# Kernel optimization log

Measured on AMD Instinct MI355X. Metric: run time of the kernel, lower is better.

Reference implementation:

```python
import jax, jax.numpy as jnp
import numpy as np


def setup_inputs() -> dict:
    key = jax.random.key(0)
    k1, k2, k3 = jax.random.split(key, 3)
    x = jax.random.normal(k1, (32, 256, 64, 64), dtype=jnp.float32)
    w = jax.random.normal(k2, (1, 1, 7, 7), dtype=jnp.float32) * (1.0 / 7.0)
    b = jax.random.normal(k3, (1,), dtype=jnp.float32) * 0.1
    return {"x": x, "w": w, "b": b}


def reference(x, w, b):
    # channel-wise mean and max pooling, keepdim -> [B,1,H,W]
    pooled = jnp.mean(x, axis=1, keepdims=True) + jnp.max(x, axis=1, keepdims=True)
    # 7x7 conv, 1->1 channel, SAME padding (pad=3)
    attn = jax.lax.conv_general_dilated(
        pooled, w,
        window_strides=(1, 1),
        padding=((3, 3), (3, 3)),
        dimension_numbers=("NCHW", "OIHW", "NCHW"),
    ) + b[None, :, None, None]
    attn = jax.nn.sigmoid(attn)
    return x * attn  # broadcast over channels
```

## Files before the change

kernel.cpp:

```cpp
#include <hip/hip_runtime.h>
#include <math.h>

#define BATCH 32
#define CH    256
#define HH    64
#define WW    64
#define HW    (HH * WW)
#define NPIX  (BATCH * HW)
#define PG    (NPIX / 4)
#define NTOT  ((size_t)BATCH * CH * HW)
#define NCHUNK 4
#define CCHUNK (CH / NCHUNK)

typedef float floatx4 __attribute__((ext_vector_type(4)));

__global__ __launch_bounds__(256) void sa_pool_partial(
    const float* __restrict__ x,
    float4* __restrict__ pSum, float4* __restrict__ pMax) {
    int t = blockIdx.x * 256 + threadIdx.x;
    int pg    = t & (PG - 1);
    int chunk = t >> 15;
    int b   = pg >> 10;
    int hwg = pg & 1023;
    const float4* p = reinterpret_cast<const float4*>(
        x + (size_t)b * CH * HW + (size_t)chunk * CCHUNK * HW) + hwg;
    float4 s = make_float4(0.f, 0.f, 0.f, 0.f);
    float4 m = make_float4(-INFINITY, -INFINITY, -INFINITY, -INFINITY);
#pragma unroll 8
    for (int c = 0; c < CCHUNK; ++c) {
        float4 v = p[c * (HW / 4)];
        s.x += v.x; s.y += v.y; s.z += v.z; s.w += v.w;
        m.x = fmaxf(m.x, v.x); m.y = fmaxf(m.y, v.y);
        m.z = fmaxf(m.z, v.z); m.w = fmaxf(m.w, v.w);
    }
    pSum[chunk * PG + pg] = s;
    pMax[chunk * PG + pg] = m;
}

__global__ __launch_bounds__(256) void sa_comb_conv(
    const float4* __restrict__ pSum, const float4* __restrict__ pMax,
    const float* __restrict__ wgt, const float* __restrict__ bias,
    float* __restrict__ attn) {
    __shared__ float pooled[22][64];
    __shared__ float wq[49];
    int bidx = blockIdx.x;
    int b = bidx >> 2;
    int s = bidx & 3;
    int t = threadIdx.x;
    if (t < 49) wq[t] = wgt[t];
    int rowbase = 16 * s - 3; if (rowbase < 0) rowbase = 0;
    int rowend  = 16 * s + 19; if (rowend > 64) rowend = 64;
    int nrows   = rowend - rowbase;
    int ngroups = nrows * 16;
    const float inv = 1.0f / (float)CH;
    for (int i = t; i < ngroups; i += 256) {
        int lr = i >> 4, cg = i & 15;
        int pg = b * 1024 + (rowbase + lr) * 16 + cg;
        float4 sv = make_float4(0.f, 0.f, 0.f, 0.f);
        float4 mv = make_float4(-INFINITY, -INFINITY, -INFINITY, -INFINITY);
#pragma unroll
        for (int c = 0; c < NCHUNK; ++c) {
            float4 a  = pSum[c * PG + pg];
            float4 bm = pMax[c * PG + pg];
            sv.x += a.x; sv.y += a.y; sv.z += a.z; sv.w += a.w;
            mv.x = fmaxf(mv.x, bm.x); mv.y = fmaxf(mv.y, bm.y);
            mv.z = fmaxf(mv.z, bm.z); mv.w = fmaxf(mv.w, bm.w);
        }
        pooled[lr][cg * 4 + 0] = sv.x * inv + mv.x;
        pooled[lr][cg * 4 + 1] = sv.y * inv + mv.y;
        pooled[lr][cg * 4 + 2] = sv.z * inv + mv.z;
        pooled[lr][cg * 4 + 3] = sv.w * inv + mv.w;
    }
    __syncthreads();
    float bv = bias[0];
    for (int i = t; i < 1024; i += 256) {
        int r = i >> 6, w = i & 63;
        int gr = 16 * s + r;
        float acc = bv;
#pragma unroll
        for (int kh = 0; kh < 7; ++kh) {
            int gr2 = gr + kh - 3;
            if (gr2 < 0 || gr2 >= HH) continue;
            int lr = gr2 - rowbase;
#pragma unroll
            for (int kw = 0; kw < 7; ++kw) {
                int w2 = w + kw - 3;
                if (w2 < 0 || w2 >= WW) continue;
                acc += pooled[lr][w2] * wq[kh * 7 + kw];
            }
        }
        attn[b * HW + gr * 64 + w] = 1.0f / (1.0f + __expf(-acc));
    }
}

__global__ __launch_bounds__(256) void sa_mul(
    const float* __restrict__ x, const float4* __restrict__ attn4,
    float* __restrict__ out) {
    int t = blockIdx.x * 256 + threadIdx.x;
    int pg = t & (PG - 1);
    int cq = t >> 15;
    int b  = pg >> 10;
    float4 a = attn4[pg];
    size_t base = (size_t)b * CH * HW + (size_t)cq * CCHUNK * HW
                + (size_t)(pg & 1023) * 4;
    const float* xp = x + base;
    float* op = out + base;
#pragma unroll 8
    for (int c = 0; c < CCHUNK; ++c) {
        float4 v = *reinterpret_cast<const float4*>(xp + (size_t)c * HW);
        floatx4 o;
        o.x = v.x * a.x; o.y = v.y * a.y; o.z = v.z * a.z; o.w = v.w * a.w;
        __builtin_nontemporal_store(o, reinterpret_cast<floatx4*>(op + (size_t)c * HW));
    }
}

extern "C" void kernel_launch(void* const* d_in, const int* in_sizes, int n_in,
                              void* d_out, int out_size, void* d_ws, size_t ws_size,
                              hipStream_t stream) {
    const float* x    = (const float*)d_in[0];
    const float* wgt  = (const float*)d_in[1];
    const float* bias = (const float*)d_in[2];
    float* out = (float*)d_out;

    float*  attn = (float*)d_ws;
    float4* pSum = reinterpret_cast<float4*>(attn + NPIX);
    float4* pMax = pSum + (size_t)NCHUNK * PG;

    sa_pool_partial<<<dim3((PG * NCHUNK) / 256), dim3(256), 0, stream>>>(
        x, pSum, pMax);
    sa_comb_conv<<<dim3(BATCH * 4), dim3(256), 0, stream>>>(
        pSum, pMax, wgt, bias, attn);
    sa_mul<<<dim3((PG * NCHUNK) / 256), dim3(256), 0, stream>>>(
        x, reinterpret_cast<const float4*>(attn), out);
}
```

Measured before the change: 82.87 us.

## Fuse channel-partial combine into pooling and fuse conv into multiply kernel

Cuts the pipeline from three kernels to two. The pooling kernel now reduces its channel chunks across warps in shared memory and writes the final pooled map directly, so the pSum/pMax partials no longer go to global memory. The second kernel recomputes the 7x7 conv and sigmoid for its own 128-pixel segment from a small halo of pooled rows, then scales x, which removes the separate attention-map pass and one launch. The cost is that each block recomputes halo rows and the pooling kernel adds a block barrier.

```diff
diff --git a/kernel.cpp b/kernel.cpp
--- a/kernel.cpp
+++ b/kernel.cpp
@@ -7,110 +7,119 @@
 #define WW    64
 #define HW    (HH * WW)
 #define NPIX  (BATCH * HW)
-#define PG    (NPIX / 4)
 #define NTOT  ((size_t)BATCH * CH * HW)
-#define NCHUNK 4
-#define CCHUNK (CH / NCHUNK)
+
+#define PIX_PER_BLK 128
+#define GRP_PER_BLK 32
+#define NCHUNK 8
+#define CCHUNK 32
+#define NBLK  (NPIX / PIX_PER_BLK)
 
 typedef float floatx4 __attribute__((ext_vector_type(4)));
 
-__global__ __launch_bounds__(256) void sa_pool_partial(
-    const float* __restrict__ x,
-    float4* __restrict__ pSum, float4* __restrict__ pMax) {
-    int t = blockIdx.x * 256 + threadIdx.x;
-    int pg    = t & (PG - 1);
-    int chunk = t >> 15;
-    int b   = pg >> 10;
-    int hwg = pg & 1023;
-    const float4* p = reinterpret_cast<const float4*>(
-        x + (size_t)b * CH * HW + (size_t)chunk * CCHUNK * HW) + hwg;
+__global__ __launch_bounds__(256) void sa_pool(
+    const float* __restrict__ x, float4* __restrict__ pooled4) {
+    __shared__ float4 sS[NCHUNK][GRP_PER_BLK];
+    __shared__ float4 sM[NCHUNK][GRP_PER_BLK];
+    int t = threadIdx.x;
+    int g = t & 31;
+    int c = t >> 5;
+    int img = blockIdx.x >> 5;
+    int seg = blockIdx.x & 31;
+    int pix0 = seg * PIX_PER_BLK;
+    const float* p = x + (size_t)img * CH * HW + (size_t)c * CCHUNK * HW
+                   + pix0 + g * 4;
     float4 s = make_float4(0.f, 0.f, 0.f, 0.f);
     float4 m = make_float4(-INFINITY, -INFINITY, -INFINITY, -INFINITY);
 #pragma unroll 8
-    for (int c = 0; c < CCHUNK; ++c) {
-        float4 v = p[c * (HW / 4)];
+    for (int i = 0; i < CCHUNK; ++i) {
+        float4 v = *reinterpret_cast<const float4*>(p + (size_t)i * HW);
         s.x += v.x; s.y += v.y; s.z += v.z; s.w += v.w;
         m.x = fmaxf(m.x, v.x); m.y = fmaxf(m.y, v.y);
         m.z = fmaxf(m.z, v.z); m.w = fmaxf(m.w, v.w);
     }
-    pSum[chunk * PG + pg] = s;
-    pMax[chunk * PG + pg] = m;
+    sS[c][g] = s;
+    sM[c][g] = m;
+    __syncthreads();
+    if (t < GRP_PER_BLK) {
+        float4 as = sS[0][t];
+        float4 am = sM[0][t];
+#pragma unroll
+        for (int cc = 1; cc < NCHUNK; ++cc) {
+            float4 bs = sS[cc][t];
+            float4 bm = sM[cc][t];
+            as.x += bs.x; as.y += bs.y; as.z += bs.z; as.w += bs.w;
+            am.x = fmaxf(am.x, bm.x); am.y = fmaxf(am.y, bm.y);
+            am.z = fmaxf(am.z, bm.z); am.w = fmaxf(am.w, bm.w);
+        }
+        const float inv = 1.0f / (float)CH;
+        float4 o;
+        o.x = as.x * inv + am.x; o.y = as.y * inv + am.y;
+        o.z = as.z * inv + am.z; o.w = as.w * inv + am.w;
+        pooled4[(img * HW + pix0) / 4 + t] = o;
+    }
 }
 
-__global__ __launch_bounds__(256) void sa_comb_conv(
-    const float4* __restrict__ pSum, const float4* __restrict__ pMax,
+__global__ __launch_bounds__(256) void sa_conv_mul(
+    const float* __restrict__ x, const float4* __restrict__ pooled4,
     const float* __restrict__ wgt, const float* __restrict__ bias,
-    float* __restrict__ attn) {
-    __shared__ float pooled[22][64];
+    float* __restrict__ out) {
+    __shared__ float pool_s[8][64];
+    __shared__ float attn_s[PIX_PER_BLK];
     __shared__ float wq[49];
-    int bidx = blockIdx.x;
-    int b = bidx >> 2;
-    int s = bidx & 3;
     int t = threadIdx.x;
+    int img = blockIdx.x >> 5;
+    int seg = blockIdx.x & 31;
+    int pix0 = seg * PIX_PER_BLK;
+    int r0 = seg * 2;
     if (t < 49) wq[t] = wgt[t];
-    int rowbase = 16 * s - 3; if (rowbase < 0) rowbase = 0;
-    int rowend  = 16 * s + 19; if (rowend > 64) rowend = 64;
-    int nrows   = rowend - rowbase;
-    int ngroups = nrows * 16;
-    const float inv = 1.0f / (float)CH;
-    for (int i = t; i < ngroups; i += 256) {
-        int lr = i >> 4, cg = i & 15;
-        int pg = b * 1024 + (rowbase + lr) * 16 + cg;
-        float4 sv = make_float4(0.f, 0.f, 0.f, 0.f);
-        float4 mv = make_float4(-INFINITY, -INFINITY, -INFINITY, -INFINITY);
-#pragma unroll
-        for (int c = 0; c < NCHUNK; ++c) {
-            float4 a  = pSum[c * PG + pg];
-            float4 bm = pMax[c * PG + pg];
-            sv.x += a.x; sv.y += a.y; sv.z += a.z; sv.w += a.w;
-            mv.x = fmaxf(mv.x, bm.x); mv.y = fmaxf(mv.y, bm.y);
-            mv.z = fmaxf(mv.z, bm.z); mv.w = fmaxf(mv.w, bm.w);
-        }
-        pooled[lr][cg * 4 + 0] = sv.x * inv + mv.x;
-        pooled[lr][cg * 4 + 1] = sv.y * inv + mv.y;
-        pooled[lr][cg * 4 + 2] = sv.z * inv + mv.z;
-        pooled[lr][cg * 4 + 3] = sv.w * inv + mv.w;
+    int lo = r0 - 3; if (lo < 0) lo = 0;
+    int hi = r0 + 4; if (hi > 63) hi = 63;
+    int nrows = hi - lo + 1;
+    if (t < nrows * 16) {
+        int lr = t >> 4, cg = t & 15;
+        float4 v = pooled4[img * (HW / 4) + (lo + lr) * 16 + cg];
+        pool_s[lr][cg * 4 + 0] = v.x;
+        pool_s[lr][cg * 4 + 1] = v.y;
+        pool_s[lr][cg * 4 + 2] = v.z;
+        pool_s[lr][cg * 4 + 3] = v.w;
     }
     __syncthreads();
-    float bv = bias[0];
-    for (int i = t; i < 1024; i += 256) {
-        int r = i >> 6, w = i & 63;
-        int gr = 16 * s + r;
-        float acc = bv;
+    if (t < PIX_PER_BLK) {
+        int r = r0 + (t >> 6);
+        int w = t & 63;
+        float acc = bias[0];
 #pragma unroll
         for (int kh = 0; kh < 7; ++kh) {
-            int gr2 = gr + kh - 3;
+            int gr2 = r + kh - 3;
             if (gr2 < 0 || gr2 >= HH) continue;
-            int lr = gr2 - rowbase;
+            int lr = gr2 - lo;
 #pragma unroll
             for (int kw = 0; kw < 7; ++kw) {
                 int w2 = w + kw - 3;
                 if (w2 < 0 || w2 >= WW) continue;
-                acc += pooled[lr][w2] * wq[kh * 7 + kw];
+                acc += pool_s[lr][w2] * wq[kh * 7 + kw];
             }
         }
-        attn[b * HW + gr * 64 + w] = 1.0f / (1.0f + __expf(-acc));
+        attn_s[t] = 1.0f / (1.0f + __expf(-acc));
     }
-}
-
-__global__ __launch_bounds__(256) void sa_mul(
-    const float* __restrict__ x, const float4* __restrict__ attn4,
-    float* __restrict__ out) {
-    int t = blockIdx.x * 256 + threadIdx.x;
-    int pg = t & (PG - 1);
-    int cq = t >> 15;
-    int b  = pg >> 10;
-    float4 a = attn4[pg];
-    size_t base = (size_t)b * CH * HW + (size_t)cq * CCHUNK * HW
-                + (size_t)(pg & 1023) * 4;
+    __syncthreads();
+    int g = t & 31;
+    int c0 = t >> 5;
+    float a0 = attn_s[g * 4 + 0];
+    float a1 = attn_s[g * 4 + 1];
+    float a2 = attn_s[g * 4 + 2];
+    float a3 = attn_s[g * 4 + 3];
+    size_t base = (size_t)img * CH * HW + (size_t)c0 * CCHUNK * HW
+                + pix0 + g * 4;
     const float* xp = x + base;
     float* op = out + base;
 #pragma unroll 8
-    for (int c = 0; c < CCHUNK; ++c) {
-        float4 v = *reinterpret_cast<const float4*>(xp + (size_t)c * HW);
+    for (int i = 0; i < CCHUNK; ++i) {
+        float4 v = *reinterpret_cast<const float4*>(xp + (size_t)i * HW);
         floatx4 o;
-        o.x = v.x * a.x; o.y = v.y * a.y; o.z = v.z * a.z; o.w = v.w * a.w;
-        __builtin_nontemporal_store(o, reinterpret_cast<floatx4*>(op + (size_t)c * HW));
+        o.x = v.x * a0; o.y = v.y * a1; o.z = v.z * a2; o.w = v.w * a3;
+        __builtin_nontemporal_store(o, reinterpret_cast<floatx4*>(op + (size_t)i * HW));
     }
 }
 
@@ -122,14 +131,8 @@
     const float* bias = (const float*)d_in[2];
     float* out = (float*)d_out;
 
-    float*  attn = (float*)d_ws;
-    float4* pSum = reinterpret_cast<float4*>(attn + NPIX);
-    float4* pMax = pSum + (size_t)NCHUNK * PG;
+    float4* pooled4 = (float4*)d_ws;
 
-    sa_pool_partial<<<dim3((PG * NCHUNK) / 256), dim3(256), 0, stream>>>(
-        x, pSum, pMax);
-    sa_comb_conv<<<dim3(BATCH * 4), dim3(256), 0, stream>>>(
-        pSum, pMax, wgt, bias, attn);
-    sa_mul<<<dim3((PG * NCHUNK) / 256), dim3(256), 0, stream>>>(
-        x, reinterpret_cast<const float4*>(attn), out);
+    sa_pool<<<dim3(NBLK), dim3(256), 0, stream>>>(x, pooled4);
+    sa_conv_mul<<<dim3(NBLK), dim3(256), 0, stream>>>(x, pooled4, wgt, bias, out);
 }
```

Result: faster. 80.38 us (-3.0%).
